# Kernel tuning notes

Measured on AMD Instinct MI355X. Metric: run time of the kernel, lower is better.

The kernel has to match this reference:

```python
import jax, jax.numpy as jnp
import numpy as np

NA = 100000   # num_authors
NP = 200000   # num_papers
D = 128       # emb_dim
E_LIKE = 600000
E_CO = 600000
B = 16384     # scoring batch
EPS = 1e-8


def setup_inputs() -> dict:
    key = jax.random.key(0)
    ks = jax.random.split(key, 8)
    author_emb = jax.random.normal(ks[0], (NA, D), dtype=jnp.float32) * 0.01
    paper_emb = jax.random.normal(ks[1], (NP, D), dtype=jnp.float32) * 0.01
    authors = jax.random.randint(ks[2], (B,), 0, NA)
    papers = jax.random.randint(ks[3], (B,), 0, NP)
    like_src = jax.random.randint(ks[4], (E_LIKE,), 0, NA)   # author -> paper ('like')
    like_dst = jax.random.randint(ks[5], (E_LIKE,), 0, NP)
    co_src = jax.random.randint(ks[6], (E_CO,), 0, NA)       # author -> author ('co')
    co_dst = jax.random.randint(ks[7], (E_CO,), 0, NA)
    return {"author_emb": author_emb, "paper_emb": paper_emb,
            "authors": authors, "papers": papers,
            "like_src": like_src, "like_dst": like_dst,
            "co_src": co_src, "co_dst": co_dst}


def _deg(ids, n):
    return jax.ops.segment_sum(jnp.ones_like(ids, dtype=jnp.float32), ids, num_segments=n)


def reference(author_emb, paper_emb, authors, papers, like_src, like_dst, co_src, co_dst):
    # degree-based self-weights (from out_degrees in the original forward)
    da = _deg(like_src, NA)                      # author out-degree on 'like'
    dp = _deg(like_dst, NP)                      # paper  out-degree on 'rev_like'
    u_sw = (1.0 - da / (da + EPS))[:, None]      # [NA, 1]
    i_sw = (1.0 - dp / (dp + EPS))[:, None]      # [NP, 1]

    # symmetric (LightGCN-style) edge normalization coefficients
    dcs = _deg(co_src, NA)
    dcd = _deg(co_dst, NA)
    co_coef = jax.lax.rsqrt(jnp.maximum(dcs[co_src] * dcd[co_dst], 1.0))[:, None]      # [E_CO, 1]
    like_coef = jax.lax.rsqrt(jnp.maximum(da[like_src] * dp[like_dst], 1.0))[:, None]  # [E_LIKE, 1]

    def co_conv(h):  # CoConv: author-author normalized message passing
        return jax.ops.segment_sum(h[co_src] * co_coef, co_dst, num_segments=NA)

    def write_conv(a, p):  # WriteConv: bipartite pass with degree self-weights
        a_out = u_sw * a + jax.ops.segment_sum(p[like_dst] * like_coef, like_src, num_segments=NA)
        p_out = i_sw * p + jax.ops.segment_sum(a[like_src] * like_coef, like_dst, num_segments=NP)
        return a_out, p_out

    # layer 1
    co_a1 = co_conv(author_emb)
    wr_a1, wr_p1 = write_conv(author_emb, paper_emb)
    a1 = 0.5 * co_a1 + 0.5 * wr_a1
    # layer 2
    co_a2 = co_conv(co_a1)
    wr_a2, _wr_p2 = write_conv(wr_a1, wr_p1)
    a2 = 0.5 * co_a2 + 0.5 * wr_a2

    # l_author = [0, 1, 2] -> sum of layer outputs
    final_author = author_emb + a1 + a2
    final_paper = paper_emb

    latest_author = final_author[authors]        # [B, D]
    latest_paper = final_paper[papers]           # [B, D]
    predict = jax.nn.sigmoid(jnp.sum(latest_author * latest_paper, axis=1))  # [B]
    return predict, latest_author, latest_paper
```

## Files before the change

kernel.cpp:

```cpp
#include <hip/hip_runtime.h>
#include <math.h>

#define NAUTH 100000
#define NPAP  200000
#define DIM   128
#define ELIKE 600000
#define ECO   600000
#define BATCH 16384
#define EPSW  1e-8f

static_assert(ELIKE == ECO, "degree kernel assumes equal edge counts");

__global__ __launch_bounds__(256) void degree_kernel(
    const int* __restrict__ like_src, const int* __restrict__ like_dst,
    const int* __restrict__ co_src,   const int* __restrict__ co_dst,
    int* __restrict__ deg_ls, int* __restrict__ deg_ld,
    int* __restrict__ deg_cs, int* __restrict__ deg_cd)
{
    int stride = gridDim.x * blockDim.x;
    for (int i = blockIdx.x * blockDim.x + threadIdx.x; i < ELIKE; i += stride) {
        atomicAdd(&deg_ls[like_src[i]], 1);
        atomicAdd(&deg_ld[like_dst[i]], 1);
        atomicAdd(&deg_cs[co_src[i]],   1);
        atomicAdd(&deg_cd[co_dst[i]],   1);
    }
}

#define SCAN_CHUNK 1024

__global__ __launch_bounds__(256) void scan_block_sums(
    const int* __restrict__ deg, int* __restrict__ bsum, int n)
{
    __shared__ int sd[256];
    int t = threadIdx.x;
    int base = blockIdx.x * SCAN_CHUNK + t * 4;
    int s = 0;
    #pragma unroll
    for (int j = 0; j < 4; ++j) { int idx = base + j; if (idx < n) s += deg[idx]; }
    sd[t] = s; __syncthreads();
    for (int o = 128; o > 0; o >>= 1) { if (t < o) sd[t] += sd[t + o]; __syncthreads(); }
    if (t == 0) bsum[blockIdx.x] = sd[0];
}

__global__ void scan_serial(int* __restrict__ bsum, int nb)
{
    if (threadIdx.x == 0 && blockIdx.x == 0) {
        int run = 0;
        for (int i = 0; i < nb; ++i) { int v = bsum[i]; bsum[i] = run; run += v; }
    }
}

__global__ __launch_bounds__(256) void scan_write_cur(
    const int* __restrict__ deg, const int* __restrict__ bsum,
    int* __restrict__ cur, int n)
{
    __shared__ int sd[256];
    int t = threadIdx.x;
    int base = blockIdx.x * SCAN_CHUNK + t * 4;
    int d[4]; int s = 0;
    #pragma unroll
    for (int j = 0; j < 4; ++j) {
        int idx = base + j;
        d[j] = (idx < n) ? deg[idx] : 0;
        s += d[j];
    }
    sd[t] = s; __syncthreads();
    for (int o = 1; o < 256; o <<= 1) {
        int v = (t >= o) ? sd[t - o] : 0;
        __syncthreads();
        sd[t] += v;
        __syncthreads();
    }
    int excl = sd[t] - s + bsum[blockIdx.x];
    #pragma unroll
    for (int j = 0; j < 4; ++j) {
        int idx = base + j;
        if (idx < n) { cur[idx] = excl; excl += d[j]; }
    }
}

__global__ __launch_bounds__(256) void placement_kernel(
    const int* __restrict__ like_src, const int* __restrict__ like_dst,
    const int* __restrict__ co_src,   const int* __restrict__ co_dst,
    const int* __restrict__ deg_ls, const int* __restrict__ deg_ld,
    const int* __restrict__ deg_cs, const int* __restrict__ deg_cd,
    int* __restrict__ cur_ls, int* __restrict__ cur_ld, int* __restrict__ cur_cd,
    int2* __restrict__ pairs_ls, int2* __restrict__ pairs_ld,
    int2* __restrict__ pairs_cd)
{
    int stride = gridDim.x * blockDim.x;
    for (int i = blockIdx.x * blockDim.x + threadIdx.x; i < ELIKE; i += stride) {
        int ls = like_src[i], ld = like_dst[i];
        float lc = 1.0f / sqrtf(fmaxf((float)deg_ls[ls] * (float)deg_ld[ld], 1.0f));
        int lcb = __float_as_int(lc);
        int s1 = atomicAdd(&cur_ls[ls], 1);
        pairs_ls[s1] = make_int2(ld, lcb);
        int s2 = atomicAdd(&cur_ld[ld], 1);
        pairs_ld[s2] = make_int2(ls, lcb);

        int cs = co_src[i], cd = co_dst[i];
        float cc = 1.0f / sqrtf(fmaxf((float)deg_cs[cs] * (float)deg_cd[cd], 1.0f));
        int s3 = atomicAdd(&cur_cd[cd], 1);
        pairs_cd[s3] = make_int2(cs, __float_as_int(cc));
    }
}

__device__ __forceinline__ void seg_acc(
    const int2* __restrict__ pairs, int start, int end, int lane,
    const float* __restrict__ src, float2& acc)
{
    for (int base = start; base < end; base += 64) {
        int m = end - base; if (m > 64) m = 64;
        int2 pr = make_int2(0, 0);
        if (lane < m) pr = pairs[base + lane];
        for (int k = 0; k < m; ++k) {
            int   g = __shfl(pr.x, k);
            float c = __int_as_float(__shfl(pr.y, k));
            float2 v = ((const float2*)(src + (size_t)g * DIM))[lane];
            acc.x += v.x * c;
            acc.y += v.y * c;
        }
    }
}

__global__ __launch_bounds__(256) void l1_author_kernel(
    const float* __restrict__ author_emb, const float* __restrict__ paper_emb,
    const int* __restrict__ cur_cd, const int* __restrict__ deg_cd,
    const int2* __restrict__ pairs_cd,
    const int* __restrict__ cur_ls, const int* __restrict__ deg_ls,
    const int2* __restrict__ pairs_ls,
    float* __restrict__ co_a1, float* __restrict__ wr_a1)
{
    int lane = threadIdx.x & 63;
    int n = blockIdx.x * (blockDim.x >> 6) + (threadIdx.x >> 6);
    if (n >= NAUTH) return;

    float2 accc = make_float2(0.f, 0.f);
    float2 accw = make_float2(0.f, 0.f);
    int ec = cur_cd[n], dc = deg_cd[n];
    seg_acc(pairs_cd, ec - dc, ec, lane, author_emb, accc);
    int el = cur_ls[n], dl = deg_ls[n];
    seg_acc(pairs_ls, el - dl, el, lane, paper_emb, accw);

    float d  = (float)dl;
    float sw = 1.0f - d / (d + EPSW);
    float2 base = ((const float2*)(author_emb + (size_t)n * DIM))[lane];
    float2 wr;
    wr.x = sw * base.x + accw.x;
    wr.y = sw * base.y + accw.y;
    ((float2*)(co_a1 + (size_t)n * DIM))[lane] = accc;
    ((float2*)(wr_a1 + (size_t)n * DIM))[lane] = wr;
}

__global__ __launch_bounds__(256) void l1_paper_kernel(
    const float* __restrict__ author_emb, const float* __restrict__ paper_emb,
    const int* __restrict__ cur_ld, const int* __restrict__ deg_ld,
    const int2* __restrict__ pairs_ld,
    float* __restrict__ wr_p1)
{
    int lane = threadIdx.x & 63;
    int n = blockIdx.x * (blockDim.x >> 6) + (threadIdx.x >> 6);
    if (n >= NPAP) return;

    float2 acc = make_float2(0.f, 0.f);
    int e = cur_ld[n], dg = deg_ld[n];
    seg_acc(pairs_ld, e - dg, e, lane, author_emb, acc);

    float d  = (float)dg;
    float sw = 1.0f - d / (d + EPSW);
    float2 base = ((const float2*)(paper_emb + (size_t)n * DIM))[lane];
    acc.x += sw * base.x;
    acc.y += sw * base.y;
    ((float2*)(wr_p1 + (size_t)n * DIM))[lane] = acc;
}

__global__ __launch_bounds__(256) void l2_author_kernel(
    const float* __restrict__ co_a1, const float* __restrict__ wr_a1,
    const float* __restrict__ wr_p1,
    const int* __restrict__ cur_cd, const int* __restrict__ deg_cd,
    const int2* __restrict__ pairs_cd,
    const int* __restrict__ cur_ls, const int* __restrict__ deg_ls,
    const int2* __restrict__ pairs_ls,
    float* __restrict__ a2buf)
{
    int lane = threadIdx.x & 63;
    int n = blockIdx.x * (blockDim.x >> 6) + (threadIdx.x >> 6);
    if (n >= NAUTH) return;

    float2 acc = make_float2(0.f, 0.f);
    int ec = cur_cd[n], dc = deg_cd[n];
    seg_acc(pairs_cd, ec - dc, ec, lane, co_a1, acc);
    int el = cur_ls[n], dl = deg_ls[n];
    seg_acc(pairs_ls, el - dl, el, lane, wr_p1, acc);

    float d  = (float)dl;
    float sw = 1.0f - d / (d + EPSW);
    float2 base = ((const float2*)(wr_a1 + (size_t)n * DIM))[lane];
    acc.x = 0.5f * (acc.x + sw * base.x);
    acc.y = 0.5f * (acc.y + sw * base.y);
    ((float2*)(a2buf + (size_t)n * DIM))[lane] = acc;
}

__global__ __launch_bounds__(256) void final_kernel(
    const float* __restrict__ author_emb, const float* __restrict__ paper_emb,
    const int* __restrict__ authors, const int* __restrict__ papers,
    const float* __restrict__ co_a1, const float* __restrict__ wr_a1,
    const float* __restrict__ a2buf,
    float* __restrict__ out_pred, float* __restrict__ out_a, float* __restrict__ out_p)
{
    int lane  = threadIdx.x & 63;
    int wpb   = blockDim.x >> 6;
    int wave0 = blockIdx.x * wpb + (threadIdx.x >> 6);
    int wstr  = gridDim.x * wpb;
    for (int b = wave0; b < BATCH; b += wstr) {
        int a = authors[b];
        int p = papers[b];
        size_t arow = (size_t)a * DIM;
        size_t prow = (size_t)p * DIM;
        float2 e  = ((const float2*)(author_emb + arow))[lane];
        float2 c1 = ((const float2*)(co_a1 + arow))[lane];
        float2 w1 = ((const float2*)(wr_a1 + arow))[lane];
        float2 a2 = ((const float2*)(a2buf + arow))[lane];
        float fx = e.x + 0.5f * c1.x + 0.5f * w1.x + a2.x;
        float fy = e.y + 0.5f * c1.y + 0.5f * w1.y + a2.y;
        float2 pp = ((const float2*)(paper_emb + prow))[lane];
        ((float2*)(out_a + (size_t)b * DIM))[lane] = make_float2(fx, fy);
        ((float2*)(out_p + (size_t)b * DIM))[lane] = pp;
        float dot = fx * pp.x + fy * pp.y;
        #pragma unroll
        for (int off = 32; off; off >>= 1) dot += __shfl_xor(dot, off);
        if (lane == 0) out_pred[b] = 1.0f / (1.0f + expf(-dot));
    }
}

extern "C" void kernel_launch(void* const* d_in, const int* in_sizes, int n_in,
                              void* d_out, int out_size, void* d_ws, size_t ws_size,
                              hipStream_t stream) {
    const float* author_emb = (const float*)d_in[0];
    const float* paper_emb  = (const float*)d_in[1];
    const int*   authors    = (const int*)d_in[2];
    const int*   papers     = (const int*)d_in[3];
    const int*   like_src   = (const int*)d_in[4];
    const int*   like_dst   = (const int*)d_in[5];
    const int*   co_src     = (const int*)d_in[6];
    const int*   co_dst     = (const int*)d_in[7];

    size_t off = 0;
    auto alloc = [&](size_t bytes) -> void* {
        void* p = (char*)d_ws + off;
        off += (bytes + 255) & ~(size_t)255;
        return p;
    };
    int* deg_ls = (int*)alloc((size_t)NAUTH * 4);
    int* deg_ld = (int*)alloc((size_t)NPAP  * 4);
    int* deg_cs = (int*)alloc((size_t)NAUTH * 4);
    int* deg_cd = (int*)alloc((size_t)NAUTH * 4);
    size_t deg_bytes = off;

    int* cur_ls = (int*)alloc((size_t)NAUTH * 4);
    int* cur_ld = (int*)alloc((size_t)NPAP  * 4);
    int* cur_cd = (int*)alloc((size_t)NAUTH * 4);
    int* bsum_ls = (int*)alloc(1024);
    int* bsum_ld = (int*)alloc(1024);
    int* bsum_cd = (int*)alloc(1024);
    int2* pairs_ls = (int2*)alloc((size_t)ELIKE * 8);
    int2* pairs_ld = (int2*)alloc((size_t)ELIKE * 8);
    int2* pairs_cd = (int2*)alloc((size_t)ECO   * 8);

    float* co_a1 = (float*)alloc((size_t)NAUTH * DIM * 4);
    float* wr_a1 = (float*)alloc((size_t)NAUTH * DIM * 4);
    float* wr_p1 = (float*)alloc((size_t)NPAP  * DIM * 4);
    float* a2buf = (float*)alloc((size_t)NAUTH * DIM * 4);

    float* out_pred = (float*)d_out;
    float* out_a    = out_pred + BATCH;
    float* out_p    = out_a + (size_t)BATCH * DIM;

    const int nb_ls = (NAUTH + SCAN_CHUNK - 1) / SCAN_CHUNK;
    const int nb_ld = (NPAP  + SCAN_CHUNK - 1) / SCAN_CHUNK;
    const int nb_cd = nb_ls;

    hipMemsetAsync(d_ws, 0, deg_bytes, stream);
    degree_kernel<<<2344, 256, 0, stream>>>(like_src, like_dst, co_src, co_dst,
                                            deg_ls, deg_ld, deg_cs, deg_cd);

    scan_block_sums<<<nb_ls, 256, 0, stream>>>(deg_ls, bsum_ls, NAUTH);
    scan_block_sums<<<nb_ld, 256, 0, stream>>>(deg_ld, bsum_ld, NPAP);
    scan_block_sums<<<nb_cd, 256, 0, stream>>>(deg_cd, bsum_cd, NAUTH);
    scan_serial<<<1, 64, 0, stream>>>(bsum_ls, nb_ls);
    scan_serial<<<1, 64, 0, stream>>>(bsum_ld, nb_ld);
    scan_serial<<<1, 64, 0, stream>>>(bsum_cd, nb_cd);
    scan_write_cur<<<nb_ls, 256, 0, stream>>>(deg_ls, bsum_ls, cur_ls, NAUTH);
    scan_write_cur<<<nb_ld, 256, 0, stream>>>(deg_ld, bsum_ld, cur_ld, NPAP);
    scan_write_cur<<<nb_cd, 256, 0, stream>>>(deg_cd, bsum_cd, cur_cd, NAUTH);

    placement_kernel<<<2344, 256, 0, stream>>>(like_src, like_dst, co_src, co_dst,
                                               deg_ls, deg_ld, deg_cs, deg_cd,
                                               cur_ls, cur_ld, cur_cd,
                                               pairs_ls, pairs_ld, pairs_cd);

    l1_author_kernel<<<(NAUTH + 3) / 4, 256, 0, stream>>>(
        author_emb, paper_emb,
        cur_cd, deg_cd, pairs_cd, cur_ls, deg_ls, pairs_ls,
        co_a1, wr_a1);
    l1_paper_kernel<<<(NPAP + 3) / 4, 256, 0, stream>>>(
        author_emb, paper_emb, cur_ld, deg_ld, pairs_ld, wr_p1);

    l2_author_kernel<<<(NAUTH + 3) / 4, 256, 0, stream>>>(
        co_a1, wr_a1, wr_p1,
        cur_cd, deg_cd, pairs_cd, cur_ls, deg_ls, pairs_ls,
        a2buf);

    final_kernel<<<4096, 256, 0, stream>>>(author_emb, paper_emb, authors, papers,
                                           co_a1, wr_a1, a2buf,
                                           out_pred, out_a, out_p);
}
```

Baseline: 825.0 us.

## Split wavefront into half-waves gathering float4 rows and merge layer-1 kernels

The segment gather now has each half of a 64-lane wavefront handle a different neighbor edge with float4 loads, two edges per half per step, then combine the halves with an xor shuffle. This raises memory-level parallelism per wave and cuts the serial edge loop length. The author and paper layer-1 kernels are fused into one launch indexed by wave id, removing a launch and the tail between them. In exchange it adds shuffle reductions, idle lanes in the epilogue, and a changed summation order.

Measured after the change: 748.9 us. 9.2% less time.

```diff
diff --git a/kernel.cpp b/kernel.cpp
--- a/kernel.cpp
+++ b/kernel.cpp
@@ -105,73 +105,105 @@
     }
 }
 
-__device__ __forceinline__ void seg_acc(
+__device__ __forceinline__ void seg_acc4(
     const int2* __restrict__ pairs, int start, int end, int lane,
-    const float* __restrict__ src, float2& acc)
+    int half, int sub, const float* __restrict__ src,
+    float4& acca, float4& accb)
 {
     for (int base = start; base < end; base += 64) {
         int m = end - base; if (m > 64) m = 64;
         int2 pr = make_int2(0, 0);
         if (lane < m) pr = pairs[base + lane];
-        for (int k = 0; k < m; ++k) {
-            int   g = __shfl(pr.x, k);
-            float c = __int_as_float(__shfl(pr.y, k));
-            float2 v = ((const float2*)(src + (size_t)g * DIM))[lane];
-            acc.x += v.x * c;
-            acc.y += v.y * c;
+        for (int k = 0; k < m; k += 4) {
+            int kk0 = k + half;
+            int kk1 = k + 2 + half;
+            int   g0 = __shfl(pr.x, kk0);
+            float c0 = __int_as_float(__shfl(pr.y, kk0));
+            int   g1 = __shfl(pr.x, kk1);
+            float c1 = __int_as_float(__shfl(pr.y, kk1));
+            if (kk0 < m) {
+                float4 v = ((const float4*)(src + (size_t)g0 * DIM))[sub];
+                acca.x += v.x * c0; acca.y += v.y * c0;
+                acca.z += v.z * c0; acca.w += v.w * c0;
+            }
+            if (kk1 < m) {
+                float4 v = ((const float4*)(src + (size_t)g1 * DIM))[sub];
+                accb.x += v.x * c1; accb.y += v.y * c1;
+                accb.z += v.z * c1; accb.w += v.w * c1;
+            }
         }
     }
 }
 
-__global__ __launch_bounds__(256) void l1_author_kernel(
+__device__ __forceinline__ float4 xh_reduce(float4 a, float4 b)
+{
+    float4 r;
+    r.x = a.x + b.x; r.y = a.y + b.y; r.z = a.z + b.z; r.w = a.w + b.w;
+    r.x += __shfl_xor(r.x, 32);
+    r.y += __shfl_xor(r.y, 32);
+    r.z += __shfl_xor(r.z, 32);
+    r.w += __shfl_xor(r.w, 32);
+    return r;
+}
+
+__global__ __launch_bounds__(256) void l1_kernel(
     const float* __restrict__ author_emb, const float* __restrict__ paper_emb,
     const int* __restrict__ cur_cd, const int* __restrict__ deg_cd,
     const int2* __restrict__ pairs_cd,
     const int* __restrict__ cur_ls, const int* __restrict__ deg_ls,
     const int2* __restrict__ pairs_ls,
-    float* __restrict__ co_a1, float* __restrict__ wr_a1)
-{
-    int lane = threadIdx.x & 63;
-    int n = blockIdx.x * (blockDim.x >> 6) + (threadIdx.x >> 6);
-    if (n >= NAUTH) return;
-
-    float2 accc = make_float2(0.f, 0.f);
-    float2 accw = make_float2(0.f, 0.f);
-    int ec = cur_cd[n], dc = deg_cd[n];
-    seg_acc(pairs_cd, ec - dc, ec, lane, author_emb, accc);
-    int el = cur_ls[n], dl = deg_ls[n];
-    seg_acc(pairs_ls, el - dl, el, lane, paper_emb, accw);
-
-    float d  = (float)dl;
-    float sw = 1.0f - d / (d + EPSW);
-    float2 base = ((const float2*)(author_emb + (size_t)n * DIM))[lane];
-    float2 wr;
-    wr.x = sw * base.x + accw.x;
-    wr.y = sw * base.y + accw.y;
-    ((float2*)(co_a1 + (size_t)n * DIM))[lane] = accc;
-    ((float2*)(wr_a1 + (size_t)n * DIM))[lane] = wr;
-}
-
-__global__ __launch_bounds__(256) void l1_paper_kernel(
-    const float* __restrict__ author_emb, const float* __restrict__ paper_emb,
     const int* __restrict__ cur_ld, const int* __restrict__ deg_ld,
     const int2* __restrict__ pairs_ld,
+    float* __restrict__ co_a1, float* __restrict__ wr_a1,
     float* __restrict__ wr_p1)
 {
     int lane = threadIdx.x & 63;
-    int n = blockIdx.x * (blockDim.x >> 6) + (threadIdx.x >> 6);
-    if (n >= NPAP) return;
-
-    float2 acc = make_float2(0.f, 0.f);
-    int e = cur_ld[n], dg = deg_ld[n];
-    seg_acc(pairs_ld, e - dg, e, lane, author_emb, acc);
-
-    float d  = (float)dg;
-    float sw = 1.0f - d / (d + EPSW);
-    float2 base = ((const float2*)(paper_emb + (size_t)n * DIM))[lane];
-    acc.x += sw * base.x;
-    acc.y += sw * base.y;
-    ((float2*)(wr_p1 + (size_t)n * DIM))[lane] = acc;
+    int half = lane >> 5;
+    int sub  = lane & 31;
+    int wid  = blockIdx.x * (blockDim.x >> 6) + (threadIdx.x >> 6);
+
+    if (wid < NAUTH) {
+        int n = wid;
+        float4 ca = make_float4(0.f,0.f,0.f,0.f), cb = ca;
+        float4 wa = ca, wb = ca;
+        int ec = cur_cd[n], dc = deg_cd[n];
+        seg_acc4(pairs_cd, ec - dc, ec, lane, half, sub, author_emb, ca, cb);
+        int el = cur_ls[n], dl = deg_ls[n];
+        seg_acc4(pairs_ls, el - dl, el, lane, half, sub, paper_emb, wa, wb);
+
+        float4 cacc = xh_reduce(ca, cb);
+        float4 wacc = xh_reduce(wa, wb);
+        if (half == 0) {
+            float d  = (float)dl;
+            float sw = 1.0f - d / (d + EPSW);
+            float4 base = ((const float4*)(author_emb + (size_t)n * DIM))[sub];
+            float4 wr;
+            wr.x = sw * base.x + wacc.x;
+            wr.y = sw * base.y + wacc.y;
+            wr.z = sw * base.z + wacc.z;
+            wr.w = sw * base.w + wacc.w;
+            ((float4*)(co_a1 + (size_t)n * DIM))[sub] = cacc;
+            ((float4*)(wr_a1 + (size_t)n * DIM))[sub] = wr;
+        }
+    } else {
+        int n = wid - NAUTH;
+        if (n >= NPAP) return;
+        float4 pa = make_float4(0.f,0.f,0.f,0.f), pb = pa;
+        int e = cur_ld[n], dg = deg_ld[n];
+        seg_acc4(pairs_ld, e - dg, e, lane, half, sub, author_emb, pa, pb);
+
+        float4 acc = xh_reduce(pa, pb);
+        if (half == 0) {
+            float d  = (float)dg;
+            float sw = 1.0f - d / (d + EPSW);
+            float4 base = ((const float4*)(paper_emb + (size_t)n * DIM))[sub];
+            acc.x += sw * base.x;
+            acc.y += sw * base.y;
+            acc.z += sw * base.z;
+            acc.w += sw * base.w;
+            ((float4*)(wr_p1 + (size_t)n * DIM))[sub] = acc;
+        }
+    }
 }
 
 __global__ __launch_bounds__(256) void l2_author_kernel(
@@ -184,21 +216,28 @@
     float* __restrict__ a2buf)
 {
     int lane = threadIdx.x & 63;
+    int half = lane >> 5;
+    int sub  = lane & 31;
     int n = blockIdx.x * (blockDim.x >> 6) + (threadIdx.x >> 6);
     if (n >= NAUTH) return;
 
-    float2 acc = make_float2(0.f, 0.f);
+    float4 aa = make_float4(0.f,0.f,0.f,0.f), ab = aa;
     int ec = cur_cd[n], dc = deg_cd[n];
-    seg_acc(pairs_cd, ec - dc, ec, lane, co_a1, acc);
+    seg_acc4(pairs_cd, ec - dc, ec, lane, half, sub, co_a1, aa, ab);
     int el = cur_ls[n], dl = deg_ls[n];
-    seg_acc(pairs_ls, el - dl, el, lane, wr_p1, acc);
-
-    float d  = (float)dl;
-    float sw = 1.0f - d / (d + EPSW);
-    float2 base = ((const float2*)(wr_a1 + (size_t)n * DIM))[lane];
-    acc.x = 0.5f * (acc.x + sw * base.x);
-    acc.y = 0.5f * (acc.y + sw * base.y);
-    ((float2*)(a2buf + (size_t)n * DIM))[lane] = acc;
+    seg_acc4(pairs_ls, el - dl, el, lane, half, sub, wr_p1, aa, ab);
+
+    float4 acc = xh_reduce(aa, ab);
+    if (half == 0) {
+        float d  = (float)dl;
+        float sw = 1.0f - d / (d + EPSW);
+        float4 base = ((const float4*)(wr_a1 + (size_t)n * DIM))[sub];
+        acc.x = 0.5f * (acc.x + sw * base.x);
+        acc.y = 0.5f * (acc.y + sw * base.y);
+        acc.z = 0.5f * (acc.z + sw * base.z);
+        acc.w = 0.5f * (acc.w + sw * base.w);
+        ((float4*)(a2buf + (size_t)n * DIM))[sub] = acc;
+    }
 }
 
 __global__ __launch_bounds__(256) void final_kernel(
@@ -299,12 +338,12 @@
                                                cur_ls, cur_ld, cur_cd,
                                                pairs_ls, pairs_ld, pairs_cd);
 
-    l1_author_kernel<<<(NAUTH + 3) / 4, 256, 0, stream>>>(
+    l1_kernel<<<(NAUTH + NPAP + 3) / 4, 256, 0, stream>>>(
         author_emb, paper_emb,
-        cur_cd, deg_cd, pairs_cd, cur_ls, deg_ls, pairs_ls,
-        co_a1, wr_a1);
-    l1_paper_kernel<<<(NPAP + 3) / 4, 256, 0, stream>>>(
-        author_emb, paper_emb, cur_ld, deg_ld, pairs_ld, wr_p1);
+        cur_cd, deg_cd, pairs_cd,
+        cur_ls, deg_ls, pairs_ls,
+        cur_ld, deg_ld, pairs_ld,
+        co_a1, wr_a1, wr_p1);
 
     l2_author_kernel<<<(NAUTH + 3) / 4, 256, 0, stream>>>(
         co_a1, wr_a1, wr_p1,
```
